# Kernel optimization log

Hardware: AMD Instinct MI355X
Metric: run time of the kernel (lower is better)

Reference implementation:

```python
import jax, jax.numpy as jnp
import numpy as np

KERNEL_SIZE = 10
CHANNELS = 3
MEAN = (KERNEL_SIZE - 1) // 2  # 4


def setup_inputs() -> dict:
    key = jax.random.key(0)
    x = jax.random.uniform(key, (32, CHANNELS, 512, 512), dtype=jnp.float32)
    return {"x": x}


def reference(x) -> jnp.ndarray:
    # (1 - x) * 0.5, then replicate pad by MEAN on H and W
    y = (1.0 - x) * 0.5
    y = jnp.pad(y, ((0, 0), (0, 0), (MEAN, MEAN), (MEAN, MEAN)), mode="edge")
    # depthwise (groups=channels) conv with all-ones 10x10 kernel, VALID padding
    # weight layout OIHW with O=CHANNELS, I=1 (feature_group_count=CHANNELS)
    w = jnp.ones((CHANNELS, 1, KERNEL_SIZE, KERNEL_SIZE), dtype=x.dtype)
    out = jax.lax.conv_general_dilated(
        y, w,
        window_strides=(1, 1),
        padding="VALID",
        dimension_numbers=("NCHW", "OIHW", "NCHW"),
        feature_group_count=CHANNELS,
    )
    return out  # [B, C, H-1, W-1]
```

## Files before the change

### kernel.cpp

```cpp
#include <hip/hip_runtime.h>


#define IMG 512
#define OUTW 511
#define KS 10
#define MEAN 4
#define SUB 8
#define TSTREAM (SUB + KS - 1)
#define NBANDS (IMG / (2 * SUB))
#define NIMG 96
#define NWG (NBANDS * NIMG)
#define CPX (NWG / 8)

__global__ __launch_bounds__(256, 4) void onedilate_kernel(
    const float* __restrict__ x, float* __restrict__ out)
{
    const int lin = blockIdx.y * NBANDS + blockIdx.x;
    const int swz = (lin & 7) * CPX + (lin >> 3);
    const int bx  = swz & (NBANDS - 1);
    const int bc  = swz >> 5;

    const int tid = threadIdx.x;
    const int j   = tid & 127;
    const int sub = __builtin_amdgcn_readfirstlane(tid >> 7);
    const int rb  = bx * (2 * SUB) + sub * SUB;

    const float* __restrict__ xim = x + (size_t)bc * (IMG * IMG);
    float* __restrict__ oim = out + (size_t)bc * (OUTW * OUTW);

    const int cbase = 4 * j;
    const int bl0 = max(cbase - 4, 0);
    const int bl2 = min(cbase + 4, IMG - 4);
    const int bl3 = min(cbase + 8, IMG - 4);
    const bool lo0 = (cbase - 4 < 0);
    const bool hi2 = (cbase + 4 > IMG - 4);
    const bool hi3 = (cbase + 8 > IMG - 4);

    float4 ring[KS];
#pragma unroll
    for (int k = 0; k < KS; ++k) ring[k] = make_float4(0.f, 0.f, 0.f, 0.f);
    float4 V = make_float4(0.f, 0.f, 0.f, 0.f);

    float4 P[2][4];

#define LOADROW(s_, d_)                                                    \
    {                                                                      \
        const int ri_ = min(max(rb + (s_) - MEAN, 0), IMG - 1);            \
        const float* __restrict__ rp_ = xim + ri_ * IMG;                   \
        P[d_][0] = *(const float4*)(rp_ + bl0);                            \
        P[d_][1] = *(const float4*)(rp_ + cbase);                          \
        P[d_][2] = *(const float4*)(rp_ + bl2);                            \
        P[d_][3] = *(const float4*)(rp_ + bl3);                            \
    }

    LOADROW(0, 0)

#pragma unroll
    for (int s = 0; s < TSTREAM; ++s) {
        const int cur = s & 1;
        float4 v0 = P[cur][0], v1 = P[cur][1], v2 = P[cur][2], v3 = P[cur][3];

        if (s + 1 < TSTREAM) LOADROW(s + 1, cur ^ 1)

        if (lo0) v0 = make_float4(v0.x, v0.x, v0.x, v0.x);
        if (hi2) v2 = make_float4(v2.w, v2.w, v2.w, v2.w);
        const float w12 = hi3 ? v3.w : v3.x;

        const float S = ((v0.x + v0.y) + (v0.z + v0.w))
                      + ((v1.x + v1.y) + (v1.z + v1.w))
                      + (v2.x + v2.y);
        const float d1  = v2.z - v0.x;
        const float d2  = v2.w - v0.y;
        const float d3  = w12  - v0.z;
        const float d12 = d1 + d2;
        float4 H;
        H.x = S;
        H.y = S + d1;
        H.z = S + d12;
        H.w = S + (d12 + d3);

        const int u = s % KS;
        V.x += H.x - ring[u].x;
        V.y += H.y - ring[u].y;
        V.z += H.z - ring[u].z;
        V.w += H.w - ring[u].w;
        ring[u] = H;

        if (s >= KS - 1) {
            const int i = rb + s - (KS - 1);
            if (i < OUTW) {
                float* op = oim + (size_t)i * OUTW + cbase;
                op[0] = fmaf(V.x, -0.5f, 50.0f);
                op[1] = fmaf(V.y, -0.5f, 50.0f);
                op[2] = fmaf(V.z, -0.5f, 50.0f);
                if (cbase + 3 < OUTW) op[3] = fmaf(V.w, -0.5f, 50.0f);
            }
        }
    }
#undef LOADROW
}

extern "C" void kernel_launch(void* const* d_in, const int* in_sizes, int n_in,
                              void* d_out, int out_size, void* d_ws, size_t ws_size,
                              hipStream_t stream) {
    const float* x = (const float*)d_in[0];
    float* out = (float*)d_out;

    dim3 block(256, 1, 1);
    dim3 grid(NBANDS, NIMG, 1);
    onedilate_kernel<<<grid, block, 0, stream>>>(x, out);
}
```

Before: 208.6 us.

## Stage 16-row input band in LDS and compute four output rows per thread

```diff
diff --git a/kernel.cpp b/kernel.cpp
--- a/kernel.cpp
+++ b/kernel.cpp
@@ -5,29 +5,53 @@
 #define OUTW 511
 #define KS 10
 #define MEAN 4
-#define SUB 8
-#define TSTREAM (SUB + KS - 1)
-#define NBANDS (IMG / (2 * SUB))
+#define SUBB 16
+#define TS (SUBB + KS - 1)
+#define ROWF4 (IMG / 4)
+#define NF4 (TS * ROWF4)
+#define NTHREADS 512
+#define NLOAD ((NF4 + NTHREADS - 1) / NTHREADS)
+#define NBANDS (IMG / SUBB)
 #define NIMG 96
 #define NWG (NBANDS * NIMG)
 #define CPX (NWG / 8)
 
-__global__ __launch_bounds__(256, 4) void onedilate_kernel(
+__global__ __launch_bounds__(NTHREADS, 6) void onedilate_kernel(
     const float* __restrict__ x, float* __restrict__ out)
 {
+    __shared__ float4 smem[NF4];
+
     const int lin = blockIdx.y * NBANDS + blockIdx.x;
     const int swz = (lin & 7) * CPX + (lin >> 3);
     const int bx  = swz & (NBANDS - 1);
     const int bc  = swz >> 5;
 
     const int tid = threadIdx.x;
-    const int j   = tid & 127;
-    const int sub = __builtin_amdgcn_readfirstlane(tid >> 7);
-    const int rb  = bx * (2 * SUB) + sub * SUB;
+    const int rb  = bx * SUBB;
 
     const float* __restrict__ xim = x + (size_t)bc * (IMG * IMG);
     float* __restrict__ oim = out + (size_t)bc * (OUTW * OUTW);
 
+    float4 t[NLOAD];
+#pragma unroll
+    for (int k = 0; k < NLOAD; ++k) {
+        const int idx = k * NTHREADS + tid;
+        if (idx < NF4) {
+            const int r  = idx >> 7;
+            const int c4 = idx & (ROWF4 - 1);
+            const int ri = min(max(rb - MEAN + r, 0), IMG - 1);
+            t[k] = *(const float4*)(xim + (size_t)ri * IMG + c4 * 4);
+        }
+    }
+#pragma unroll
+    for (int k = 0; k < NLOAD; ++k) {
+        const int idx = k * NTHREADS + tid;
+        if (idx < NF4) smem[idx] = t[k];
+    }
+    __syncthreads();
+
+    const int j  = tid & 127;
+    const int rg = tid >> 7;
     const int cbase = 4 * j;
     const int bl0 = max(cbase - 4, 0);
     const int bl2 = min(cbase + 4, IMG - 4);
@@ -36,32 +60,20 @@
     const bool hi2 = (cbase + 4 > IMG - 4);
     const bool hi3 = (cbase + 8 > IMG - 4);
 
-    float4 ring[KS];
-#pragma unroll
-    for (int k = 0; k < KS; ++k) ring[k] = make_float4(0.f, 0.f, 0.f, 0.f);
-    float4 V = make_float4(0.f, 0.f, 0.f, 0.f);
+    const float* sf = (const float*)smem;
+    float4 a0 = make_float4(0.f, 0.f, 0.f, 0.f);
+    float4 a1 = a0, a2 = a0, a3 = a0;
 
-    float4 P[2][4];
-
-#define LOADROW(s_, d_)                                                    \
-    {                                                                      \
-        const int ri_ = min(max(rb + (s_) - MEAN, 0), IMG - 1);            \
-        const float* __restrict__ rp_ = xim + ri_ * IMG;                   \
-        P[d_][0] = *(const float4*)(rp_ + bl0);                            \
-        P[d_][1] = *(const float4*)(rp_ + cbase);                          \
-        P[d_][2] = *(const float4*)(rp_ + bl2);                            \
-        P[d_][3] = *(const float4*)(rp_ + bl3);                            \
-    }
-
-    LOADROW(0, 0)
+#define ACC4(A) { A.x += H.x; A.y += H.y; A.z += H.z; A.w += H.w; }
 
 #pragma unroll
-    for (int s = 0; s < TSTREAM; ++s) {
-        const int cur = s & 1;
-        float4 v0 = P[cur][0], v1 = P[cur][1], v2 = P[cur][2], v3 = P[cur][3];
-
-        if (s + 1 < TSTREAM) LOADROW(s + 1, cur ^ 1)
-
+    for (int sl = 0; sl < 13; ++sl) {
+        const int s = rg * 4 + sl;
+        const float* rp = sf + s * IMG;
+        float4 v0 = *(const float4*)(rp + bl0);
+        float4 v1 = *(const float4*)(rp + cbase);
+        float4 v2 = *(const float4*)(rp + bl2);
+        float4 v3 = *(const float4*)(rp + bl3);
         if (lo0) v0 = make_float4(v0.x, v0.x, v0.x, v0.x);
         if (hi2) v2 = make_float4(v2.w, v2.w, v2.w, v2.w);
         const float w12 = hi3 ? v3.w : v3.x;
@@ -79,25 +91,28 @@
         H.z = S + d12;
         H.w = S + (d12 + d3);
 
-        const int u = s % KS;
-        V.x += H.x - ring[u].x;
-        V.y += H.y - ring[u].y;
-        V.z += H.z - ring[u].z;
-        V.w += H.w - ring[u].w;
-        ring[u] = H;
+        if (sl <= 9)             ACC4(a0)
+        if (sl >= 1 && sl <= 10) ACC4(a1)
+        if (sl >= 2 && sl <= 11) ACC4(a2)
+        if (sl >= 3)             ACC4(a3)
+    }
+#undef ACC4
 
-        if (s >= KS - 1) {
-            const int i = rb + s - (KS - 1);
-            if (i < OUTW) {
-                float* op = oim + (size_t)i * OUTW + cbase;
-                op[0] = fmaf(V.x, -0.5f, 50.0f);
-                op[1] = fmaf(V.y, -0.5f, 50.0f);
-                op[2] = fmaf(V.z, -0.5f, 50.0f);
-                if (cbase + 3 < OUTW) op[3] = fmaf(V.w, -0.5f, 50.0f);
-            }
-        }
-    }
-#undef LOADROW
+    const int i0 = rb + rg * 4;
+#define STORE(ro, A)                                                       \
+    { const int i = i0 + (ro);                                             \
+      if (i < OUTW) {                                                      \
+          float* op = oim + (size_t)i * OUTW + cbase;                      \
+          op[0] = fmaf(A.x, -0.5f, 50.0f);                                 \
+          op[1] = fmaf(A.y, -0.5f, 50.0f);                                 \
+          op[2] = fmaf(A.z, -0.5f, 50.0f);                                 \
+          if (cbase + 3 < OUTW) op[3] = fmaf(A.w, -0.5f, 50.0f);           \
+      } }
+    STORE(0, a0)
+    STORE(1, a1)
+    STORE(2, a2)
+    STORE(3, a3)
+#undef STORE
 }
 
 extern "C" void kernel_launch(void* const* d_in, const int* in_sizes, int n_in,
@@ -106,7 +121,7 @@
     const float* x = (const float*)d_in[0];
     float* out = (float*)d_out;
 
-    dim3 block(256, 1, 1);
+    dim3 block(NTHREADS, 1, 1);
     dim3 grid(NBANDS, NIMG, 1);
     onedilate_kernel<<<grid, block, 0, stream>>>(x, out);
 }
```

Result: slower. 254.6 us (+22.1%).

## Restructure to wave-per-row with vertical sums shared via lane shuffles

Applied to the files above, without the earlier changes.

```diff
diff --git a/kernel.cpp b/kernel.cpp
--- a/kernel.cpp
+++ b/kernel.cpp
@@ -3,16 +3,32 @@
 
 #define IMG 512
 #define OUTW 511
-#define KS 10
 #define MEAN 4
-#define SUB 8
-#define TSTREAM (SUB + KS - 1)
-#define NBANDS (IMG / (2 * SUB))
+#define ROWSPW 4
+#define NTHREADS 256
+#define ROWSPB 16
+#define NBANDS (IMG / ROWSPB)
 #define NIMG 96
 #define NWG (NBANDS * NIMG)
 #define CPX (NWG / 8)
 
-__global__ __launch_bounds__(256, 4) void onedilate_kernel(
+__device__ __forceinline__ float4 f4add(float4 a, float4 b) {
+    return make_float4(a.x + b.x, a.y + b.y, a.z + b.z, a.w + b.w);
+}
+__device__ __forceinline__ float4 f4slide(float4 v, float4 add, float4 sub) {
+    return make_float4(v.x + add.x - sub.x, v.y + add.y - sub.y,
+                       v.z + add.z - sub.z, v.w + add.w - sub.w);
+}
+__device__ __forceinline__ float4 shflup1(float4 v) {
+    return make_float4(__shfl_up(v.x, 1, 64), __shfl_up(v.y, 1, 64),
+                       __shfl_up(v.z, 1, 64), __shfl_up(v.w, 1, 64));
+}
+__device__ __forceinline__ float4 shfldn1(float4 v) {
+    return make_float4(__shfl_down(v.x, 1, 64), __shfl_down(v.y, 1, 64),
+                       __shfl_down(v.z, 1, 64), __shfl_down(v.w, 1, 64));
+}
+
+__global__ __launch_bounds__(NTHREADS) void onedilate_kernel(
     const float* __restrict__ x, float* __restrict__ out)
 {
     const int lin = blockIdx.y * NBANDS + blockIdx.x;
@@ -20,84 +36,75 @@
     const int bx  = swz & (NBANDS - 1);
     const int bc  = swz >> 5;
 
-    const int tid = threadIdx.x;
-    const int j   = tid & 127;
-    const int sub = __builtin_amdgcn_readfirstlane(tid >> 7);
-    const int rb  = bx * (2 * SUB) + sub * SUB;
+    const int tid  = threadIdx.x;
+    const int lane = tid & 63;
+    const int wid  = tid >> 6;
+    const int i0   = bx * ROWSPB + wid * ROWSPW;
 
     const float* __restrict__ xim = x + (size_t)bc * (IMG * IMG);
     float* __restrict__ oim = out + (size_t)bc * (OUTW * OUTW);
+    const float* cp = xim + lane * 8;
 
-    const int cbase = 4 * j;
-    const int bl0 = max(cbase - 4, 0);
-    const int bl2 = min(cbase + 4, IMG - 4);
-    const int bl3 = min(cbase + 8, IMG - 4);
-    const bool lo0 = (cbase - 4 < 0);
-    const bool hi2 = (cbase + 4 > IMG - 4);
-    const bool hi3 = (cbase + 8 > IMG - 4);
-
-    float4 ring[KS];
+    float4 a[13], b[13];
 #pragma unroll
-    for (int k = 0; k < KS; ++k) ring[k] = make_float4(0.f, 0.f, 0.f, 0.f);
-    float4 V = make_float4(0.f, 0.f, 0.f, 0.f);
-
-    float4 P[2][4];
-
-#define LOADROW(s_, d_)                                                    \
-    {                                                                      \
-        const int ri_ = min(max(rb + (s_) - MEAN, 0), IMG - 1);            \
-        const float* __restrict__ rp_ = xim + ri_ * IMG;                   \
-        P[d_][0] = *(const float4*)(rp_ + bl0);                            \
-        P[d_][1] = *(const float4*)(rp_ + cbase);                          \
-        P[d_][2] = *(const float4*)(rp_ + bl2);                            \
-        P[d_][3] = *(const float4*)(rp_ + bl3);                            \
+    for (int k = 0; k < 13; ++k) {
+        const int ri = min(max(i0 - MEAN + k, 0), IMG - 1);
+        const float* rp = cp + (size_t)ri * IMG;
+        a[k] = *(const float4*)rp;
+        b[k] = *(const float4*)(rp + 4);
     }
 
-    LOADROW(0, 0)
+    float4 va = f4add(f4add(f4add(f4add(a[0], a[1]), f4add(a[2], a[3])),
+                            f4add(f4add(a[4], a[5]), f4add(a[6], a[7]))),
+                      f4add(a[8], a[9]));
+    float4 vb = f4add(f4add(f4add(f4add(b[0], b[1]), f4add(b[2], b[3])),
+                            f4add(f4add(b[4], b[5]), f4add(b[6], b[7]))),
+                      f4add(b[8], b[9]));
 
 #pragma unroll
-    for (int s = 0; s < TSTREAM; ++s) {
-        const int cur = s & 1;
-        float4 v0 = P[cur][0], v1 = P[cur][1], v2 = P[cur][2], v3 = P[cur][3];
+    for (int r = 0; r < ROWSPW; ++r) {
+        if (r > 0) {
+            va = f4slide(va, a[9 + r], a[r - 1]);
+            vb = f4slide(vb, b[9 + r], b[r - 1]);
+        }
+        float4 L = shflup1(vb);
+        float4 R = shfldn1(va);
+        float  rx = __shfl_down(vb.x, 1, 64);
+        if (lane == 0)  L = make_float4(va.x, va.x, va.x, va.x);
+        if (lane == 63) { R = make_float4(vb.w, vb.w, vb.w, vb.w);
+                          rx = vb.w; }
 
-        if (s + 1 < TSTREAM) LOADROW(s + 1, cur ^ 1)
+        const float S = ((L.x + L.y) + (L.z + L.w))
+                      + ((va.x + va.y) + (va.z + va.w))
+                      + (vb.x + vb.y);
+        const float h0 = S;
+        const float h1 = h0 + vb.z - L.x;
+        const float h2 = h1 + vb.w - L.y;
+        const float h3 = h2 + R.x  - L.z;
+        const float h4 = h3 + R.y  - L.w;
+        const float h5 = h4 + R.z  - va.x;
+        const float h6 = h5 + R.w  - va.y;
+        const float h7 = h6 + rx   - va.z;
 
-        if (lo0) v0 = make_float4(v0.x, v0.x, v0.x, v0.x);
-        if (hi2) v2 = make_float4(v2.w, v2.w, v2.w, v2.w);
-        const float w12 = hi3 ? v3.w : v3.x;
-
-        const float S = ((v0.x + v0.y) + (v0.z + v0.w))
-                      + ((v1.x + v1.y) + (v1.z + v1.w))
-                      + (v2.x + v2.y);
-        const float d1  = v2.z - v0.x;
-        const float d2  = v2.w - v0.y;
-        const float d3  = w12  - v0.z;
-        const float d12 = d1 + d2;
-        float4 H;
-        H.x = S;
-        H.y = S + d1;
-        H.z = S + d12;
-        H.w = S + (d12 + d3);
-
-        const int u = s % KS;
-        V.x += H.x - ring[u].x;
-        V.y += H.y - ring[u].y;
-        V.z += H.z - ring[u].z;
-        V.w += H.w - ring[u].w;
-        ring[u] = H;
-
-        if (s >= KS - 1) {
-            const int i = rb + s - (KS - 1);
-            if (i < OUTW) {
-                float* op = oim + (size_t)i * OUTW + cbase;
-                op[0] = fmaf(V.x, -0.5f, 50.0f);
-                op[1] = fmaf(V.y, -0.5f, 50.0f);
-                op[2] = fmaf(V.z, -0.5f, 50.0f);
-                if (cbase + 3 < OUTW) op[3] = fmaf(V.w, -0.5f, 50.0f);
+        const int i = i0 + r;
+        if (i < OUTW) {
+            float* op = oim + (size_t)i * OUTW + lane * 8;
+            *(float4*)op = make_float4(fmaf(h0, -0.5f, 50.0f),
+                                       fmaf(h1, -0.5f, 50.0f),
+                                       fmaf(h2, -0.5f, 50.0f),
+                                       fmaf(h3, -0.5f, 50.0f));
+            if (lane < 63) {
+                *(float4*)(op + 4) = make_float4(fmaf(h4, -0.5f, 50.0f),
+                                                 fmaf(h5, -0.5f, 50.0f),
+                                                 fmaf(h6, -0.5f, 50.0f),
+                                                 fmaf(h7, -0.5f, 50.0f));
+            } else {
+                op[4] = fmaf(h4, -0.5f, 50.0f);
+                op[5] = fmaf(h5, -0.5f, 50.0f);
+                op[6] = fmaf(h6, -0.5f, 50.0f);
             }
         }
     }
-#undef LOADROW
 }
 
 extern "C" void kernel_launch(void* const* d_in, const int* in_sizes, int n_in,
@@ -106,7 +113,7 @@
     const float* x = (const float*)d_in[0];
     float* out = (float*)d_out;
 
-    dim3 block(256, 1, 1);
+    dim3 block(NTHREADS, 1, 1);
     dim3 grid(NBANDS, NIMG, 1);
     onedilate_kernel<<<grid, block, 0, stream>>>(x, out);
 }
```

After: 185.4 us. 1.13x faster.
